# Kernel optimization log

Measured on AMD Instinct MI355X. Metric: run time of the kernel, lower is better.

The kernel has to match this reference:

```python
import jax, jax.numpy as jnp
import numpy as np
from jax import lax

RESI_RATIO = 0.5  # abs(quant_resi=-0.5)
BETA = 0.25


def setup_inputs() -> dict:
    key = jax.random.key(0)
    k1, k2, k3, k4 = jax.random.split(key, 4)
    B, C, T, H, W = 2, 32, 8, 32, 32
    V = 8192
    f_BCTHW = jax.random.normal(k1, (B, C, T, H, W), dtype=jnp.float32)
    emb_weight = jax.random.normal(k2, (V, C), dtype=jnp.float32)
    conv_w = jax.random.normal(k3, (C, C, 3, 3, 3), dtype=jnp.float32) * 0.02
    conv_b = jax.random.normal(k4, (C,), dtype=jnp.float32) * 0.02
    return {"f_BCTHW": f_BCTHW, "emb_weight": emb_weight, "conv_w": conv_w, "conv_b": conv_b}


def _mse(a, b):
    d = a - b
    return jnp.mean(d * d)


def reference(f_BCTHW, emb_weight, conv_w, conv_b):
    f = f_BCTHW.astype(jnp.float32)
    B, C, T, H, W = f.shape
    V = emb_weight.shape[0]

    # ---- nearest-codebook assignment (vocab_norm=False path) ----
    # query uses detached f (stop_gradient) exactly as torch .detach()
    q = lax.stop_gradient(f).transpose(0, 2, 3, 4, 1).reshape(-1, C)  # [N, C]
    emb_sg = lax.stop_gradient(emb_weight)
    # ||q||^2 + ||e||^2 - 2 q.e  (addmm_ with alpha=-2, beta=1)
    dist = (jnp.sum(q * q, axis=1, keepdims=True)
            + jnp.sum(emb_sg * emb_sg, axis=1)
            - 2.0 * (q @ emb_sg.T))  # [N, V]
    idx_N = jnp.argmin(dist, axis=1)  # [N] int

    # ---- usage stats (bincount) ----
    counts = jnp.zeros((V,), jnp.float32).at[idx_N].add(1.0)
    prob = counts / jnp.sum(counts)
    vocab_usage = jnp.mean((prob > (0.01 / V)).astype(jnp.float32)) * 100.0

    # ---- embedding gather + residual conv blend ----
    fh = emb_weight[idx_N].reshape(B, T, H, W, C).transpose(0, 4, 1, 2, 3)  # [B,C,T,H,W]
    conv = lax.conv_general_dilated(
        fh, conv_w, window_strides=(1, 1, 1), padding='SAME',
        dimension_numbers=('NCDHW', 'OIDHW', 'NCDHW'))
    conv = conv + conv_b[None, :, None, None, None]
    fh = fh * (1.0 - RESI_RATIO) + conv * RESI_RATIO

    # ---- VQ loss + straight-through estimator ----
    vq_loss = BETA * _mse(lax.stop_gradient(fh), f) + _mse(fh, lax.stop_gradient(f))
    fhat = lax.stop_gradient(fh - f) + f

    return fhat, vq_loss, vocab_usage
```

## Files before the change

kernel.cpp:

```cpp
#include <hip/hip_runtime.h>

#define NQ    16384
#define CDIM  32
#define VSZ   8192
#define PLANE 8192
#define BSTR  262144
#define NEL   524288
#define MARGIN 0.010f
#define NSEG  32
#define GUARD 1088

typedef unsigned long long u64;
typedef unsigned int u32;
typedef unsigned short u16;
using f32x4 = __attribute__((ext_vector_type(4))) float;
using s16x8 = __attribute__((ext_vector_type(8))) short;

__device__ __forceinline__ u32 flip_bits(u32 b) {
    return (b & 0x80000000u) ? ~b : (b | 0x80000000u);
}
__device__ __forceinline__ float unflip_val(u32 b) {
    u32 u = (b & 0x80000000u) ? (b ^ 0x80000000u) : ~b;
    return __uint_as_float(u);
}
__device__ __forceinline__ u16 bf16_rne(float x) {
    u32 u = __float_as_uint(x);
    return (u16)((u + 0x7fffu + ((u >> 16) & 1u)) >> 16);
}

__global__ void k_prep(const float* __restrict__ f, const float* __restrict__ emb,
                       const float* __restrict__ cw,
                       u16* __restrict__ EFh, u16* __restrict__ EFl,
                       u16* __restrict__ QFh, u16* __restrict__ QFl,
                       u16* __restrict__ WFh, u16* __restrict__ WFl,
                       float* __restrict__ enorm, int* __restrict__ counts,
                       float* __restrict__ loss_sum, int* __restrict__ uct) {
    int t = blockIdx.x * 256 + threadIdx.x;
    if (t < 32768) {
        int tile = t >> 6, l = t & 63;
        int row = tile * 16 + (l & 15);
        int k0 = (l >> 4) * 8;
        const float* src = emb + row * CDIM + k0;
        s16x8 vh, vl;
#pragma unroll
        for (int i = 0; i < 8; ++i) {
            float v = src[i];
            u16 hb = bf16_rne(v);
            float hf = __uint_as_float(((u32)hb) << 16);
            vh[i] = (short)hb;
            vl[i] = (short)bf16_rne(v - hf);
        }
        *(s16x8*)(EFh + t * 8) = vh;
        *(s16x8*)(EFl + t * 8) = vl;
    } else if (t < 98304) {
        int t2 = t - 32768;
        int st = t2 >> 6, l = t2 & 63;
        int n = st * 16 + (l & 15);
        int k0 = (l >> 4) * 8;
        int b = n >> 13, p = n & (PLANE - 1);
        const float* fq = f + b * BSTR + p;
        s16x8 vh, vl;
#pragma unroll
        for (int i = 0; i < 8; ++i) {
            float v = -2.0f * fq[(k0 + i) * PLANE];
            u16 hb = bf16_rne(v);
            float hf = __uint_as_float(((u32)hb) << 16);
            vh[i] = (short)hb;
            vl[i] = (short)bf16_rne(v - hf);
        }
        *(s16x8*)(QFh + t2 * 8) = vh;
        *(s16x8*)(QFl + t2 * 8) = vl;
    } else if (t < 106496) {
        int j = t - 98304;
        const float4* row = (const float4*)(emb + j * CDIM);
        float s = 0.f;
#pragma unroll
        for (int r = 0; r < 8; ++r) {
            float4 v = row[r];
            s += v.x * v.x + v.y * v.y + v.z * v.z + v.w * v.w;
        }
        enorm[j] = s;
        counts[j] = 0;
        if (j == 0) { *loss_sum = 0.f; *uct = 0; }
    } else if (t < 109952) {
        int i = t - 106496;
        int nt = i >> 6, l = i & 63;
        int col = nt * 16 + (l & 15);
        int co = col & 31, u = col >> 5;
        int k0 = (l >> 4) * 8;
        s16x8 vh, vl;
#pragma unroll
        for (int j = 0; j < 8; ++j) {
            int ci = k0 + j;
            float v = cw[co * 864 + ci * 27 + u];
            u16 hb = bf16_rne(v);
            float hf = __uint_as_float(((u32)hb) << 16);
            vh[j] = (short)hb;
            vl[j] = (short)bf16_rne(v - hf);
        }
        *(s16x8*)(WFh + i * 8) = vh;
        *(s16x8*)(WFl + i * 8) = vl;
    }
}

__global__ __launch_bounds__(64) void k_mfma3(
    const u16* __restrict__ QFh, const u16* __restrict__ QFl,
    const u16* __restrict__ EFh, const u16* __restrict__ EFl,
    const float* __restrict__ enorm,
    u64* __restrict__ PARTK, float* __restrict__ PARTM2) {
    const int l = threadIdx.x;
    const int lq = (l >> 4) * 4;
    const int wq = blockIdx.x >> 5, seg = blockIdx.x & 31;

    s16x8 qh[4], ql[4];
#pragma unroll
    for (int s = 0; s < 4; ++s) {
        int st = wq * 4 + s;
        qh[s] = *(const s16x8*)(QFh + (st * 64 + l) * 8);
        ql[s] = *(const s16x8*)(QFl + (st * 64 + l) * 8);
    }
    float m1v[4] = {1e30f, 1e30f, 1e30f, 1e30f};
    float m2v[4] = {1e30f, 1e30f, 1e30f, 1e30f};
    int   m1i[4] = {0, 0, 0, 0};

#pragma unroll 2
    for (int t = 0; t < 16; ++t) {
        int tile = seg * 16 + t;
        s16x8 ah = *(const s16x8*)(EFh + (tile * 64 + l) * 8);
        s16x8 al = *(const s16x8*)(EFl + (tile * 64 + l) * 8);
        f32x4 en = *(const f32x4*)(enorm + tile * 16 + lq);
        int bc = tile * 16 + lq;
#pragma unroll
        for (int s = 0; s < 4; ++s) {
            f32x4 acc = __builtin_amdgcn_mfma_f32_16x16x32_bf16(ah, qh[s], en, 0, 0, 0);
            acc = __builtin_amdgcn_mfma_f32_16x16x32_bf16(ah, ql[s], acc, 0, 0, 0);
            acc = __builtin_amdgcn_mfma_f32_16x16x32_bf16(al, qh[s], acc, 0, 0, 0);
#pragma unroll
            for (int r = 0; r < 4; ++r) {
                float v = acc[r];
                bool lt = v < m1v[s];
                float m2c = fminf(m2v[s], v);
                m2v[s] = lt ? m1v[s] : m2c;
                m1i[s] = lt ? (bc + r) : m1i[s];
                m1v[s] = fminf(m1v[s], v);
            }
        }
    }
#pragma unroll
    for (int s = 0; s < 4; ++s) {
        u64 key = ((u64)flip_bits(__float_as_uint(m1v[s])) << 32) | (u32)m1i[s];
        float m2 = m2v[s];
#pragma unroll
        for (int off = 16; off <= 32; off <<= 1) {
            u64 ko = __shfl_xor(key, off, 64);
            float m2o = __shfl_xor(m2, off, 64);
            u64 kmax = ko > key ? ko : key;
            m2 = fminf(fminf(m2, m2o), unflip_val((u32)(kmax >> 32)));
            key = ko < key ? ko : key;
        }
        if (l < 16) {
            int q = wq * 64 + s * 16 + l;
            PARTK[seg * NQ + q] = key;
            PARTM2[seg * NQ + q] = m2;
        }
    }
}

__global__ void k_final(const u64* __restrict__ PARTK, const float* __restrict__ PARTM2,
                        int* __restrict__ out_idx, int* __restrict__ counts,
                        int* __restrict__ uct, int* __restrict__ ulist) {
    int q = blockIdx.x * 256 + threadIdx.x;
    u64 K = PARTK[q]; float M2 = PARTM2[q];
#pragma unroll
    for (int s = 1; s < NSEG; ++s) {
        u64 k = PARTK[s * NQ + q]; float m2 = PARTM2[s * NQ + q];
        u64 kmax = k > K ? k : K;
        M2 = fminf(fminf(M2, m2), unflip_val((u32)(kmax >> 32)));
        K = k < K ? k : K;
    }
    int idx = (int)(K & 0xffffffffull);
    out_idx[q] = idx;
    float m1 = unflip_val((u32)(K >> 32));
    if (M2 - m1 > MARGIN) {
        atomicAdd(&counts[idx], 1);
    } else {
        int p = atomicAdd(uct, 1);
        ulist[p] = q;
    }
}

__global__ __launch_bounds__(256) void k_exact(
    const int* __restrict__ ulist, const int* __restrict__ uct,
    const float* __restrict__ f, const float* __restrict__ emb,
    const float* __restrict__ enorm, int* __restrict__ out_idx,
    int* __restrict__ counts) {
    __shared__ u64 wred[4][2];
    const int tid = threadIdx.x;
    const int uc = *uct;
    for (int base = blockIdx.x * 2; base < uc; base += 256) {
        int nq = uc - base; if (nq > 2) nq = 2;
        int q0 = ulist[base];
        int q1 = (nq > 1) ? ulist[base + 1] : q0;
        float qv0[CDIM], qv1[CDIM];
        {
            const float* f0 = f + (q0 >> 13) * BSTR + (q0 & (PLANE - 1));
            const float* f1 = f + (q1 >> 13) * BSTR + (q1 & (PLANE - 1));
#pragma unroll
            for (int c = 0; c < CDIM; ++c) {
                qv0[c] = -2.0f * f0[c * PLANE];
                qv1[c] = -2.0f * f1[c * PLANE];
            }
        }
        u64 k0 = ~0ull, k1 = ~0ull;
        for (int jj = 0; jj < 32; ++jj) {
            int j = tid + 256 * jj;
            const float4* er = (const float4*)(emb + j * CDIM);
            float d0 = enorm[j], d1 = d0;
#pragma unroll
            for (int c4 = 0; c4 < 8; ++c4) {
                float4 v = er[c4];
                d0 = fmaf(qv0[c4 * 4 + 0], v.x, d0); d0 = fmaf(qv0[c4 * 4 + 1], v.y, d0);
                d0 = fmaf(qv0[c4 * 4 + 2], v.z, d0); d0 = fmaf(qv0[c4 * 4 + 3], v.w, d0);
                d1 = fmaf(qv1[c4 * 4 + 0], v.x, d1); d1 = fmaf(qv1[c4 * 4 + 1], v.y, d1);
                d1 = fmaf(qv1[c4 * 4 + 2], v.z, d1); d1 = fmaf(qv1[c4 * 4 + 3], v.w, d1);
            }
            u64 nk0 = ((u64)flip_bits(__float_as_uint(d0)) << 32) | (u32)j;
            u64 nk1 = ((u64)flip_bits(__float_as_uint(d1)) << 32) | (u32)j;
            if (nk0 < k0) k0 = nk0;
            if (nk1 < k1) k1 = nk1;
        }
#pragma unroll
        for (int off = 1; off <= 32; off <<= 1) {
            u64 o0 = __shfl_xor(k0, off, 64); if (o0 < k0) k0 = o0;
            u64 o1 = __shfl_xor(k1, off, 64); if (o1 < k1) k1 = o1;
        }
        if ((tid & 63) == 0) { wred[tid >> 6][0] = k0; wred[tid >> 6][1] = k1; }
        __syncthreads();
        if (tid == 0) {
            u64 b0 = wred[0][0], b1 = wred[0][1];
#pragma unroll
            for (int w = 1; w < 4; ++w) {
                if (wred[w][0] < b0) b0 = wred[w][0];
                if (wred[w][1] < b1) b1 = wred[w][1];
            }
            int i0 = (int)(b0 & 0xffffffffull);
            out_idx[q0] = i0; atomicAdd(&counts[i0], 1);
            if (nq > 1) {
                int i1 = (int)(b1 & 0xffffffffull);
                out_idx[q1] = i1; atomicAdd(&counts[i1], 1);
            }
        }
        __syncthreads();
    }
}

__global__ void k_fh2(const int* __restrict__ idx, const float* __restrict__ emb,
                      u16* __restrict__ FH2h, u16* __restrict__ FH2l) {
    int t = blockIdx.x * 256 + threadIdx.x;
    if (t < NQ) {
        int id = idx[t];
        const float4* e = (const float4*)(emb + id * CDIM);
        s16x8 vh[4], vl[4];
#pragma unroll
        for (int r = 0; r < 8; ++r) {
            float4 v = e[r];
            float vv[4] = {v.x, v.y, v.z, v.w};
#pragma unroll
            for (int j = 0; j < 4; ++j) {
                int q = r * 4 + j;
                u16 hb = bf16_rne(vv[j]);
                float hf = __uint_as_float(((u32)hb) << 16);
                vh[q >> 3][q & 7] = (short)hb;
                vl[q >> 3][q & 7] = (short)bf16_rne(vv[j] - hf);
            }
        }
        u16* dh_ = FH2h + t * CDIM;
        u16* dl_ = FH2l + t * CDIM;
#pragma unroll
        for (int r = 0; r < 4; ++r) {
            *(s16x8*)(dh_ + r * 8) = vh[r];
            *(s16x8*)(dl_ + r * 8) = vl[r];
        }
    } else {
        int g = t - NQ;
        int r = g / 1088, off = (g % 1088) * 16;
        u32* dst;
        if (r == 0)      dst = (u32*)(FH2h - GUARD * CDIM);
        else if (r == 1) dst = (u32*)(FH2h + NQ * CDIM);
        else if (r == 2) dst = (u32*)(FH2l - GUARD * CDIM);
        else             dst = (u32*)(FH2l + NQ * CDIM);
#pragma unroll
        for (int i = 0; i < 16; ++i) dst[off + i] = 0;
    }
}

__global__ __launch_bounds__(256) void k_convm(
    const u16* __restrict__ FH2h, const u16* __restrict__ FH2l,
    const u16* __restrict__ WFh, const u16* __restrict__ WFl,
    const int* __restrict__ idx, const float* __restrict__ emb,
    const float* __restrict__ bias, const float* __restrict__ f,
    float* __restrict__ out, float* __restrict__ loss_sum) {
    const int l = threadIdx.x & 63;
    const int w = blockIdx.x * 4 + (threadIdx.x >> 6);
    const int ntile = w >> 1, cot = w & 1;
    const int co = cot * 16 + (l & 15);
    const int k0 = (l >> 4) * 8;

    const int nA = ntile * 16 + (l & 15);
    const int pA = nA & (PLANE - 1);
    const int tA = pA >> 10, hA = (pA >> 5) & 31, wA = pA & 31;
    const u16* pAh = FH2h + nA * CDIM + k0;
    const u16* pAl = FH2l + nA * CDIM + k0;

    f32x4 acc;
    {
        float bv = bias[co];
        acc[0] = bv; acc[1] = bv; acc[2] = bv; acc[3] = bv;
    }
    const s16x8 zf = {0, 0, 0, 0, 0, 0, 0, 0};
#pragma unroll
    for (int u = 0; u < 27; ++u) {
        const int dt = u / 9 - 1, dh = (u / 3) % 3 - 1, dw = u % 3 - 1;
        const int du = dt * 1024 + dh * 32 + dw;
        bool ok = ((unsigned)(tA + dt) < 8u) && ((unsigned)(hA + dh) < 32u) &&
                  ((unsigned)(wA + dw) < 32u);
        s16x8 ah = *(const s16x8*)(pAh + du * CDIM);
        s16x8 al = *(const s16x8*)(pAl + du * CDIM);
        if (!ok) { ah = zf; al = zf; }
        int nt = 2 * u + cot;
        s16x8 bh = *(const s16x8*)(WFh + (nt * 64 + l) * 8);
        s16x8 bl = *(const s16x8*)(WFl + (nt * 64 + l) * 8);
        acc = __builtin_amdgcn_mfma_f32_16x16x32_bf16(ah, bh, acc, 0, 0, 0);
        acc = __builtin_amdgcn_mfma_f32_16x16x32_bf16(ah, bl, acc, 0, 0, 0);
        acc = __builtin_amdgcn_mfma_f32_16x16x32_bf16(al, bh, acc, 0, 0, 0);
    }

    const int n0 = ntile * 16 + (l >> 4) * 4;
    const int b = n0 >> 13, p0 = n0 & (PLANE - 1);
    const long fb = (long)b * BSTR + (long)co * PLANE + p0;
    const float4 f4 = *(const float4*)(f + fb);
    const int4 iv = *(const int4*)(idx + n0);
    float o0 = 0.5f * emb[iv.x * CDIM + co] + 0.5f * acc[0];
    float o1 = 0.5f * emb[iv.y * CDIM + co] + 0.5f * acc[1];
    float o2 = 0.5f * emb[iv.z * CDIM + co] + 0.5f * acc[2];
    float o3 = 0.5f * emb[iv.w * CDIM + co] + 0.5f * acc[3];
    float4 o4 = {o0, o1, o2, o3};
    *(float4*)(out + fb) = o4;
    float d0 = o0 - f4.x, d1 = o1 - f4.y, d2 = o2 - f4.z, d3 = o3 - f4.w;
    float s = fmaf(d0, d0, fmaf(d1, d1, fmaf(d2, d2, d3 * d3)));
#pragma unroll
    for (int off = 32; off > 0; off >>= 1) s += __shfl_down(s, off, 64);
    if (l == 0) atomicAdd(loss_sum, s);
}

__global__ void k_scalars(const int* __restrict__ counts,
                          const float* __restrict__ loss_sum, float* __restrict__ out) {
    int tid = threadIdx.x;
    int used = 0;
#pragma unroll
    for (int r = 0; r < 32; ++r) used += (counts[tid + 256 * r] > 0) ? 1 : 0;
#pragma unroll
    for (int off = 32; off > 0; off >>= 1) used += __shfl_down(used, off, 64);
    __shared__ int us[4];
    if ((tid & 63) == 0) us[tid >> 6] = used;
    __syncthreads();
    if (tid == 0) {
        int u = us[0] + us[1] + us[2] + us[3];
        out[NEL + 0] = 1.25f * (*loss_sum) / (float)NEL;
        out[NEL + 1] = ((float)u / (float)VSZ) * 100.0f;
    }
}

extern "C" void kernel_launch(void* const* d_in, const int* in_sizes, int n_in,
                              void* d_out, int out_size, void* d_ws, size_t ws_size,
                              hipStream_t stream) {
    const float* f      = (const float*)d_in[0];
    const float* emb    = (const float*)d_in[1];
    const float* conv_w = (const float*)d_in[2];
    const float* conv_b = (const float*)d_in[3];
    float* out = (float*)d_out;
    float* ws = (float*)d_ws;

    float* enorm    = ws;
    int*   counts   = (int*)(ws + 8192);
    int*   idxb     = (int*)(ws + 16384);
    float* loss_sum = ws + 32768;
    int*   uct      = (int*)(ws + 32769);
    int*   ulist    = (int*)(ws + 32772);
    u16*   EFh      = (u16*)(ws + 49408);
    u16*   EFl      = (u16*)(ws + 180480);
    u16*   QFh      = (u16*)(ws + 311552);
    u16*   QFl      = (u16*)(ws + 573696);
    u16*   WFh      = (u16*)(ws + 835840);
    u16*   WFl      = (u16*)(ws + 842752);
    u64*   PARTK    = (u64*)(ws + 849664);
    float* PARTM2   = ws + 1898240;
    u16*   FH2h     = (u16*)(ws + 849664)  + GUARD * CDIM;
    u16*   FH2l     = (u16*)(ws + 1146624) + GUARD * CDIM;

    k_prep   <<<430, 256, 0, stream>>>(f, emb, conv_w, EFh, EFl, QFh, QFl,
                                       WFh, WFl, enorm, counts, loss_sum, uct);
    k_mfma3  <<<8192, 64, 0, stream>>>(QFh, QFl, EFh, EFl, enorm, PARTK, PARTM2);
    k_final  <<<64, 256, 0, stream>>>(PARTK, PARTM2, idxb, counts, uct, ulist);
    k_exact  <<<128, 256, 0, stream>>>(ulist, uct, f, emb, enorm, idxb, counts);
    k_fh2    <<<81, 256, 0, stream>>>(idxb, emb, FH2h, FH2l);
    k_convm  <<<512, 256, 0, stream>>>(FH2h, FH2l, WFh, WFl, idxb, emb,
                                       conv_b, f, out, loss_sum);
    k_scalars<<<1, 256, 0, stream>>>(counts, loss_sum, out);
}
```

Measured before the change: 190.9 us.

## Split conv 27-tap reduction across three waves with LDS partial-sum combine

The conv kernel now gives each (tile, channel-half) its own block of three waves, one per temporal offset. Each wave accumulates 9 taps into three independent MFMA accumulators, and the partial sums are combined in shared memory before the epilogue. This shortens each wave's serial MFMA dependency chain and quadruples the number of blocks for more latency hiding. The cost is an LDS round trip, a block barrier and two idle waves during the epilogue. A 'done' counter is also added and zeroed but is not used yet.

```diff
diff --git a/kernel.cpp b/kernel.cpp
--- a/kernel.cpp
+++ b/kernel.cpp
@@ -34,7 +34,8 @@
                        u16* __restrict__ QFh, u16* __restrict__ QFl,
                        u16* __restrict__ WFh, u16* __restrict__ WFl,
                        float* __restrict__ enorm, int* __restrict__ counts,
-                       float* __restrict__ loss_sum, int* __restrict__ uct) {
+                       float* __restrict__ loss_sum, int* __restrict__ uct,
+                       int* __restrict__ done) {
     int t = blockIdx.x * 256 + threadIdx.x;
     if (t < 32768) {
         int tile = t >> 6, l = t & 63;
@@ -81,7 +82,7 @@
         }
         enorm[j] = s;
         counts[j] = 0;
-        if (j == 0) { *loss_sum = 0.f; *uct = 0; }
+        if (j == 0) { *loss_sum = 0.f; *uct = 0; *done = 0; }
     } else if (t < 109952) {
         int i = t - 106496;
         int nt = i >> 6, l = i & 63;
@@ -294,15 +295,16 @@
     }
 }
 
-__global__ __launch_bounds__(256) void k_convm(
+__global__ __launch_bounds__(192) void k_convm2(
     const u16* __restrict__ FH2h, const u16* __restrict__ FH2l,
     const u16* __restrict__ WFh, const u16* __restrict__ WFl,
     const int* __restrict__ idx, const float* __restrict__ emb,
     const float* __restrict__ bias, const float* __restrict__ f,
     float* __restrict__ out, float* __restrict__ loss_sum) {
+    __shared__ float part[3][64][4];
     const int l = threadIdx.x & 63;
-    const int w = blockIdx.x * 4 + (threadIdx.x >> 6);
-    const int ntile = w >> 1, cot = w & 1;
+    const int wv = threadIdx.x >> 6;
+    const int ntile = blockIdx.x >> 1, cot = blockIdx.x & 1;
     const int co = cot * 16 + (l & 15);
     const int k0 = (l >> 4) * 8;
 
@@ -312,38 +314,47 @@
     const u16* pAh = FH2h + nA * CDIM + k0;
     const u16* pAl = FH2l + nA * CDIM + k0;
 
-    f32x4 acc;
-    {
-        float bv = bias[co];
-        acc[0] = bv; acc[1] = bv; acc[2] = bv; acc[3] = bv;
-    }
+    const int ddt = wv - 1;
+    const bool okt = ((unsigned)(tA + ddt) < 8u);
+
+    f32x4 a0 = {0.f, 0.f, 0.f, 0.f}, a1 = a0, a2 = a0;
     const s16x8 zf = {0, 0, 0, 0, 0, 0, 0, 0};
 #pragma unroll
-    for (int u = 0; u < 27; ++u) {
-        const int dt = u / 9 - 1, dh = (u / 3) % 3 - 1, dw = u % 3 - 1;
-        const int du = dt * 1024 + dh * 32 + dw;
-        bool ok = ((unsigned)(tA + dt) < 8u) && ((unsigned)(hA + dh) < 32u) &&
-                  ((unsigned)(wA + dw) < 32u);
+    for (int v = 0; v < 9; ++v) {
+        const int dh = v / 3 - 1, dw = v % 3 - 1;
+        const int u = wv * 9 + v;
+        const int du = ddt * 1024 + dh * 32 + dw;
+        bool ok = okt && ((unsigned)(hA + dh) < 32u) && ((unsigned)(wA + dw) < 32u);
         s16x8 ah = *(const s16x8*)(pAh + du * CDIM);
         s16x8 al = *(const s16x8*)(pAl + du * CDIM);
         if (!ok) { ah = zf; al = zf; }
         int nt = 2 * u + cot;
         s16x8 bh = *(const s16x8*)(WFh + (nt * 64 + l) * 8);
         s16x8 bl = *(const s16x8*)(WFl + (nt * 64 + l) * 8);
-        acc = __builtin_amdgcn_mfma_f32_16x16x32_bf16(ah, bh, acc, 0, 0, 0);
-        acc = __builtin_amdgcn_mfma_f32_16x16x32_bf16(ah, bl, acc, 0, 0, 0);
-        acc = __builtin_amdgcn_mfma_f32_16x16x32_bf16(al, bh, acc, 0, 0, 0);
-    }
+        a0 = __builtin_amdgcn_mfma_f32_16x16x32_bf16(ah, bh, a0, 0, 0, 0);
+        a1 = __builtin_amdgcn_mfma_f32_16x16x32_bf16(ah, bl, a1, 0, 0, 0);
+        a2 = __builtin_amdgcn_mfma_f32_16x16x32_bf16(al, bh, a2, 0, 0, 0);
+    }
+#pragma unroll
+    for (int r = 0; r < 4; ++r) part[wv][l][r] = a0[r] + a1[r] + a2[r];
+    __syncthreads();
+    if (wv != 0) return;
+
+    f32x4 acc;
+#pragma unroll
+    for (int r = 0; r < 4; ++r)
+        acc[r] = part[0][l][r] + part[1][l][r] + part[2][l][r];
+    const float bv = bias[co];
 
     const int n0 = ntile * 16 + (l >> 4) * 4;
     const int b = n0 >> 13, p0 = n0 & (PLANE - 1);
     const long fb = (long)b * BSTR + (long)co * PLANE + p0;
     const float4 f4 = *(const float4*)(f + fb);
     const int4 iv = *(const int4*)(idx + n0);
-    float o0 = 0.5f * emb[iv.x * CDIM + co] + 0.5f * acc[0];
-    float o1 = 0.5f * emb[iv.y * CDIM + co] + 0.5f * acc[1];
-    float o2 = 0.5f * emb[iv.z * CDIM + co] + 0.5f * acc[2];
-    float o3 = 0.5f * emb[iv.w * CDIM + co] + 0.5f * acc[3];
+    float o0 = 0.5f * emb[iv.x * CDIM + co] + 0.5f * (acc[0] + bv);
+    float o1 = 0.5f * emb[iv.y * CDIM + co] + 0.5f * (acc[1] + bv);
+    float o2 = 0.5f * emb[iv.z * CDIM + co] + 0.5f * (acc[2] + bv);
+    float o3 = 0.5f * emb[iv.w * CDIM + co] + 0.5f * (acc[3] + bv);
     float4 o4 = {o0, o1, o2, o3};
     *(float4*)(out + fb) = o4;
     float d0 = o0 - f4.x, d1 = o1 - f4.y, d2 = o2 - f4.z, d3 = o3 - f4.w;
@@ -386,6 +397,7 @@
     int*   idxb     = (int*)(ws + 16384);
     float* loss_sum = ws + 32768;
     int*   uct      = (int*)(ws + 32769);
+    int*   done     = (int*)(ws + 32770);
     int*   ulist    = (int*)(ws + 32772);
     u16*   EFh      = (u16*)(ws + 49408);
     u16*   EFl      = (u16*)(ws + 180480);
@@ -399,12 +411,12 @@
     u16*   FH2l     = (u16*)(ws + 1146624) + GUARD * CDIM;
 
     k_prep   <<<430, 256, 0, stream>>>(f, emb, conv_w, EFh, EFl, QFh, QFl,
-                                       WFh, WFl, enorm, counts, loss_sum, uct);
+                                       WFh, WFl, enorm, counts, loss_sum, uct, done);
     k_mfma3  <<<8192, 64, 0, stream>>>(QFh, QFl, EFh, EFl, enorm, PARTK, PARTM2);
     k_final  <<<64, 256, 0, stream>>>(PARTK, PARTM2, idxb, counts, uct, ulist);
     k_exact  <<<128, 256, 0, stream>>>(ulist, uct, f, emb, enorm, idxb, counts);
     k_fh2    <<<81, 256, 0, stream>>>(idxb, emb, FH2h, FH2l);
-    k_convm  <<<512, 256, 0, stream>>>(FH2h, FH2l, WFh, WFl, idxb, emb,
-                                       conv_b, f, out, loss_sum);
+    k_convm2 <<<2048, 192, 0, stream>>>(FH2h, FH2l, WFh, WFl, idxb, emb,
+                                        conv_b, f, out, loss_sum);
     k_scalars<<<1, 256, 0, stream>>>(counts, loss_sum, out);
 }
```

After: 185.9 us. 2.6% less time.
